# Kernel tuning notes

Measured on AMD Instinct MI355X. Metric: run time of the kernel, lower is better.

The kernel has to match this reference:

```python
import jax, jax.numpy as jnp
import numpy as np

B, NS, NT, C = 32, 1000, 100, 256
LAMBDA_GIOU, LAMBDA_L1 = 10.0, 1.0


def _lsa(cost):
    """Hungarian / Jonker-Volgenant shortest-augmenting-path (numpy, O(n^2 m)).
    Matches scipy.optimize.linear_sum_assignment for rectangular matrices."""
    cost = np.asarray(cost, dtype=np.float64)
    transposed = cost.shape[0] > cost.shape[1]
    if transposed:
        cost = cost.T
    n, m = cost.shape  # n <= m
    INF = np.inf
    u = np.zeros(n + 1)
    v = np.zeros(m + 1)
    p = np.zeros(m + 1, dtype=np.int64)   # p[j] = row (1-based) assigned to col j
    way = np.zeros(m + 1, dtype=np.int64)
    for i in range(1, n + 1):
        p[0] = i
        j0 = 0
        minv = np.full(m + 1, INF)
        used = np.zeros(m + 1, dtype=bool)
        while True:
            used[j0] = True
            i0 = p[j0]
            cur = cost[i0 - 1, :] - u[i0] - v[1:]
            free = ~used[1:]
            better = free & (cur < minv[1:])
            minv[1:][better] = cur[better]
            way[1:][better] = j0
            masked = np.where(free, minv[1:], INF)
            j1 = int(np.argmin(masked)) + 1
            delta = masked[j1 - 1]
            u[p[used]] += delta
            v[used] -= delta
            minv[~used] -= delta
            j0 = j1
            if p[j0] == 0:
                break
        while j0:
            j1 = way[j0]
            p[j0] = p[j1]
            j0 = j1
    rows = p[1:] - 1
    cols = np.arange(m)
    keep = rows >= 0
    rows, cols = rows[keep], cols[keep]
    if transposed:
        rows, cols = cols, rows
    order = np.argsort(rows)
    return rows[order], cols[order]


def _pairwise_cost(logits, classes, sb, tb):
    """Per-batch (Ns,Nt) cost = CE(logits_s, class_t) + 10*(1-GIoU(box_s, box_t)) + L1mean."""
    Bc, Ns, Cd = logits.shape
    Nt = classes.shape[1]
    # Cross entropy: logsumexp over classes minus logit at target class (identical
    # math to the torch expand+flatten CE, without the Ns*Nt*C copy).
    lse = jax.nn.logsumexp(logits, axis=-1)  # (B,Ns)
    picked = jnp.take_along_axis(
        logits, jnp.broadcast_to(classes[:, None, :], (Bc, Ns, Nt)), axis=2)  # (B,Ns,Nt)
    ce = lse[:, :, None] - picked
    # Pairwise GIoU (boxes in xyxy)
    s = sb[:, :, None, :]  # (B,Ns,1,4)
    t = tb[:, None, :, :]  # (B,1,Nt,4)
    ix1 = jnp.maximum(s[..., 0], t[..., 0])
    iy1 = jnp.maximum(s[..., 1], t[..., 1])
    ix2 = jnp.minimum(s[..., 2], t[..., 2])
    iy2 = jnp.minimum(s[..., 3], t[..., 3])
    inter = jnp.clip(ix2 - ix1, 0.0) * jnp.clip(iy2 - iy1, 0.0)
    area_s = (s[..., 2] - s[..., 0]) * (s[..., 3] - s[..., 1])
    area_t = (t[..., 2] - t[..., 0]) * (t[..., 3] - t[..., 1])
    union = area_s + area_t - inter
    iou = inter / union
    cx1 = jnp.minimum(s[..., 0], t[..., 0])
    cy1 = jnp.minimum(s[..., 1], t[..., 1])
    cx2 = jnp.maximum(s[..., 2], t[..., 2])
    cy2 = jnp.maximum(s[..., 3], t[..., 3])
    carea = (cx2 - cx1) * (cy2 - cy1)
    giou = iou - (carea - union) / carea
    l1 = jnp.abs(s - t).mean(axis=-1)  # (B,Ns,Nt)
    return ce + LAMBDA_GIOU * (1.0 - giou) + LAMBDA_L1 * l1


def _valid_boxes(key, b, n):
    p = jax.random.uniform(key, (b, n, 2, 2), dtype=jnp.float32)
    lo = p.min(axis=2)
    hi = p.max(axis=2)
    return jnp.concatenate([lo, hi], axis=-1)  # (b,n,4) xyxy, x1<x2, y1<y2


def setup_inputs() -> dict:
    key = jax.random.key(0)
    k1, k2, k3, k4 = jax.random.split(key, 4)
    return {
        "source_class_logits": jax.random.normal(k1, (B, NS, C), dtype=jnp.float32),
        "target_classes": jax.random.randint(k2, (B, NT), 0, C, dtype=jnp.int32),
        "source_boxes": _valid_boxes(k3, B, NS),
        "target_boxes": _valid_boxes(k4, B, NT),
    }


def reference(source_class_logits, target_classes, source_boxes, target_boxes):
    cost = _pairwise_cost(source_class_logits, target_classes, source_boxes, target_boxes)
    cost_np = np.asarray(cost)
    rows_l, cols_l = [], []
    for b in range(cost_np.shape[0]):  # assignment is inherently per-matrix / host-side
        r, c = _lsa(cost_np[b])
        rows_l.append(r)
        cols_l.append(c)
    rows = jnp.asarray(np.stack(rows_l))  # (B, min(Ns,Nt))
    cols = jnp.asarray(np.stack(cols_l))
    bidx = jnp.arange(cost.shape[0])[:, None]
    return cost[bidx, rows, cols].mean(axis=1)  # (B,)
```

## Files before the change

kernel.cpp:

```cpp
#include <hip/hip_runtime.h>
#include <math.h>

#define NSRC 1000
#define NTGT 100
#define NCLS 256
#define NB   32
#define NSP  1024
#define PAD_IDX(j) ((j) + ((j) >> 4))
#define LDSN (NSP + (NSP >> 4))

__global__ __launch_bounds__(256) void lse_kernel(const float* __restrict__ logits,
                                                  float* __restrict__ lse) {
    int wid  = threadIdx.x >> 6;
    int lane = threadIdx.x & 63;
    int row0 = blockIdx.x * 32 + wid * 8;
    #pragma unroll 2
    for (int r = 0; r < 8; ++r) {
        int row = row0 + r;
        float4 v4 = reinterpret_cast<const float4*>(logits + (size_t)row * NCLS)[lane];
        float m = fmaxf(fmaxf(v4.x, v4.y), fmaxf(v4.z, v4.w));
        #pragma unroll
        for (int off = 32; off >= 1; off >>= 1) m = fmaxf(m, __shfl_xor(m, off));
        float s = expf(v4.x - m) + expf(v4.y - m) + expf(v4.z - m) + expf(v4.w - m);
        #pragma unroll
        for (int off = 32; off >= 1; off >>= 1) s += __shfl_xor(s, off);
        if (lane == 0) lse[row] = m + logf(s);
    }
}

__global__ __launch_bounds__(256) void cost_kernel(const float* __restrict__ logits,
                                                   const int*   __restrict__ tcls,
                                                   const float* __restrict__ sbox,
                                                   const float* __restrict__ tbox,
                                                   const float* __restrict__ lse,
                                                   float*       __restrict__ cost,
                                                   float*       __restrict__ urow_g,
                                                   int*         __restrict__ jmin_g) {
    int b  = blockIdx.x & 31;
    int t  = blockIdx.x >> 5;
    int bt = b * NTGT + t;
    int cls = tcls[bt];
    float4 tb = reinterpret_cast<const float4*>(tbox)[bt];
    float area_t = (tb.z - tb.x) * (tb.w - tb.y);
    float* crow = cost + (size_t)bt * NSP;
    float m = 1e38f; int mi = 0x7fffffff;
    for (int s = threadIdx.x; s < NSP; s += 256) {
        if (s >= NSRC) { crow[s] = 1e30f; continue; }
        int gs = b * NSRC + s;
        float4 sb = reinterpret_cast<const float4*>(sbox)[gs];
        float ce = lse[gs] - logits[(size_t)gs * NCLS + cls];
        float ix1 = fmaxf(sb.x, tb.x), iy1 = fmaxf(sb.y, tb.y);
        float ix2 = fminf(sb.z, tb.z), iy2 = fminf(sb.w, tb.w);
        float inter = fmaxf(ix2 - ix1, 0.f) * fmaxf(iy2 - iy1, 0.f);
        float area_s = (sb.z - sb.x) * (sb.w - sb.y);
        float uni = area_s + area_t - inter;
        float iou = inter / uni;
        float cx1 = fminf(sb.x, tb.x), cy1 = fminf(sb.y, tb.y);
        float cx2 = fmaxf(sb.z, tb.z), cy2 = fmaxf(sb.w, tb.w);
        float carea = (cx2 - cx1) * (cy2 - cy1);
        float giou = iou - (carea - uni) / carea;
        float l1 = 0.25f * (fabsf(sb.x - tb.x) + fabsf(sb.y - tb.y) +
                            fabsf(sb.z - tb.z) + fabsf(sb.w - tb.w));
        float c = ce + 10.0f * (1.0f - giou) + l1;
        crow[s] = c;
        if (c < m) { m = c; mi = s; }
    }
    #pragma unroll
    for (int off = 32; off >= 1; off >>= 1) {
        float om = __shfl_xor(m, off);
        int   oi = __shfl_xor(mi, off);
        if (om < m || (om == m && oi < mi)) { m = om; mi = oi; }
    }
    __shared__ float smin[4];
    __shared__ int   sidx[4];
    int wid = threadIdx.x >> 6, lane = threadIdx.x & 63;
    if (lane == 0) { smin[wid] = m; sidx[wid] = mi; }
    __syncthreads();
    if (threadIdx.x == 0) {
        #pragma unroll
        for (int w = 1; w < 4; ++w) {
            float om = smin[w]; int oi = sidx[w];
            if (om < m || (om == m && oi < mi)) { m = om; mi = oi; }
        }
        urow_g[bt] = m;
        jmin_g[bt] = mi;
    }
}

__global__ __launch_bounds__(64) void lsa_kernel(const float* __restrict__ cost,
                                                 const float* __restrict__ urow_g,
                                                 const int*   __restrict__ jmin_g,
                                                 float* __restrict__ out) {
    int b    = blockIdx.x;
    int lane = threadIdx.x;
    const float* C = cost + (size_t)b * NTGT * NSP;
    __shared__ int   way[LDSN];
    __shared__ int   pcol[LDSN];
    __shared__ float uu[LDSN];
    __shared__ float urow[NTGT];
    __shared__ int   jmin[NTGT];
    __shared__ int   done[NTGT];
    for (int t = lane; t < LDSN; t += 64) { pcol[t] = -1; uu[t] = 0.f; way[t] = 0x7fffffff; }
    for (int t = lane; t < NTGT; t += 64) {
        urow[t] = urow_g[b * NTGT + t];
        jmin[t] = jmin_g[b * NTGT + t];
    }
    float v[16], d[16];
    #pragma unroll
    for (int k = 0; k < 16; ++k) v[k] = 0.f;
    int base = lane * 16;
    __syncthreads();

    for (int r = lane; r < NTGT; r += 64) atomicMin(&way[PAD_IDX(jmin[r])], r);
    __syncthreads();
    for (int r = lane; r < NTGT; r += 64) {
        int j = jmin[r];
        int w = (way[PAD_IDX(j)] == r) ? 1 : 0;
        done[r] = w;
        if (w) { pcol[PAD_IDX(j)] = r; uu[PAD_IDX(j)] = urow[r]; }
    }
    __syncthreads();

    for (int i = 0; i < NTGT; ++i) {
        if (done[i]) continue;
        float ui = urow[i];
        {
            const float4* row4 = reinterpret_cast<const float4*>(C + (size_t)i * NSP + base);
            #pragma unroll
            for (int q = 0; q < 4; ++q) {
                float4 c4 = row4[q];
                d[4*q+0] = c4.x - ui - v[4*q+0];
                d[4*q+1] = c4.y - ui - v[4*q+1];
                d[4*q+2] = c4.z - ui - v[4*q+2];
                d[4*q+3] = c4.w - ui - v[4*q+3];
            }
        }
        #pragma unroll
        for (int k = 0; k < 16; ++k) way[PAD_IDX(base + k)] = -1;
        unsigned int used = 0;
        float Df = 0.f;
        int jf = -1;

        for (int it = 0; it < NTGT + 3; ++it) {
            float lmin = 1e38f;
            #pragma unroll
            for (int k = 0; k < 16; ++k) {
                float val = ((used >> k) & 1u) ? 1e38f : d[k];
                lmin = fminf(lmin, val);
            }
            float wmin = lmin;
            #pragma unroll
            for (int off = 32; off >= 1; off >>= 1) wmin = fminf(wmin, __shfl_xor(wmin, off));
            unsigned long long msk = __ballot(lmin == wmin);
            int src = __ffsll(msk) - 1;
            int myk = -1;
            #pragma unroll
            for (int k = 15; k >= 0; --k)
                if (!((used >> k) & 1u) && d[k] == wmin) myk = k;
            int j0 = __shfl(base + myk, src);
            if (j0 < 0) break;
            int pj0 = pcol[PAD_IDX(j0)];
            if (pj0 < 0) { Df = wmin; jf = j0; break; }
            if ((j0 >> 4) == lane) used |= 1u << (j0 & 15);
            float uref = uu[PAD_IDX(j0)];
            float sft  = wmin - uref;
            const float4* rr = reinterpret_cast<const float4*>(C + (size_t)pj0 * NSP + base);
            float cr[16];
            #pragma unroll
            for (int q = 0; q < 4; ++q) {
                float4 c4 = rr[q];
                cr[4*q+0] = c4.x; cr[4*q+1] = c4.y; cr[4*q+2] = c4.z; cr[4*q+3] = c4.w;
            }
            #pragma unroll
            for (int k = 0; k < 16; ++k) {
                float cand = sft + cr[k] - v[k];
                bool upd = (cand < d[k]) && !((used >> k) & 1u);
                if (upd) { d[k] = cand; way[PAD_IDX(base + k)] = j0; }
            }
        }

        if (jf >= 0) {
            #pragma unroll
            for (int k = 0; k < 16; ++k) {
                if ((used >> k) & 1u) {
                    float diff = Df - d[k];
                    v[k] -= diff;
                    uu[PAD_IDX(base + k)] += diff;
                }
            }
        }
        __syncthreads();
        if (lane == 0 && jf >= 0) {
            int j = jf;
            for (int g = 0; g < NSP; ++g) {
                int jp = way[PAD_IDX(j)];
                if (jp < 0) { pcol[PAD_IDX(j)] = i; uu[PAD_IDX(j)] = ui + Df; break; }
                pcol[PAD_IDX(j)] = pcol[PAD_IDX(jp)];
                uu[PAD_IDX(j)]   = uu[PAD_IDX(jp)];
                j = jp;
            }
        }
        __syncthreads();
    }

    float acc = 0.f;
    #pragma unroll
    for (int k = 0; k < 16; ++k) {
        int j = base + k;
        if (j < NSRC) {
            int r = pcol[PAD_IDX(j)];
            if (r >= 0) acc += C[(size_t)r * NSP + j];
        }
    }
    #pragma unroll
    for (int off = 32; off >= 1; off >>= 1) acc += __shfl_xor(acc, off);
    if (lane == 0) out[b] = acc * (1.0f / NTGT);
}

extern "C" void kernel_launch(void* const* d_in, const int* in_sizes, int n_in,
                              void* d_out, int out_size, void* d_ws, size_t ws_size,
                              hipStream_t stream) {
    const float* logits = (const float*)d_in[0];
    const int*   tcls   = (const int*)  d_in[1];
    const float* sbox   = (const float*)d_in[2];
    const float* tbox   = (const float*)d_in[3];
    float* out = (float*)d_out;

    float* lse    = (float*)d_ws;
    float* cost   = lse + 32768;
    float* urow_g = cost + (size_t)NB * NTGT * NSP;
    int*   jmin_g = (int*)(urow_g + NB * NTGT);

    lse_kernel <<<1000,      256, 0, stream>>>(logits, lse);
    cost_kernel<<<NB * NTGT, 256, 0, stream>>>(logits, tcls, sbox, tbox, lse, cost,
                                               urow_g, jmin_g);
    lsa_kernel <<<NB,        64,  0, stream>>>(cost, urow_g, jmin_g, out);
}
```

Baseline: 148.6 us.

## Add auction-style augmenting row reduction before shortest-path LSA phase

Adds a queue-driven augmenting row reduction pass, as in Jonker-Volgenant, after the initial column-min greedy assignment. Each unassigned row finds its best and second-best reduced cost by wavefront shuffle, takes the best column, lowers that column's price, and pushes any displaced row back onto the queue, for at most 400 steps. The aim is to assign most rows cheaply so the expensive per-row shortest augmenting path loop runs fewer times. The cost is extra serialized steps with a block barrier each, and a risk to optimality or correctness if the dual variables become inconsistent.

```diff
diff --git a/kernel.cpp b/kernel.cpp
--- a/kernel.cpp
+++ b/kernel.cpp
@@ -100,6 +100,7 @@
     __shared__ float urow[NTGT];
     __shared__ int   jmin[NTGT];
     __shared__ int   done[NTGT];
+    __shared__ int   queue[512];
     for (int t = lane; t < LDSN; t += 64) { pcol[t] = -1; uu[t] = 0.f; way[t] = 0x7fffffff; }
     for (int t = lane; t < NTGT; t += 64) {
         urow[t] = urow_g[b * NTGT + t];
@@ -118,6 +119,54 @@
         int w = (way[PAD_IDX(j)] == r) ? 1 : 0;
         done[r] = w;
         if (w) { pcol[PAD_IDX(j)] = r; uu[PAD_IDX(j)] = urow[r]; }
+    }
+    __syncthreads();
+
+    int qh = 0, qt = 0;
+    for (int r = 0; r < NTGT; ++r) {
+        if (!done[r]) { if (lane == 0) queue[qt] = r; qt++; }
+    }
+    __syncthreads();
+    int steps = 0;
+    while (qh < qt && steps < 400) {
+        ++steps;
+        int i = queue[qh++];
+        const float4* row4 = reinterpret_cast<const float4*>(C + (size_t)i * NSP + base);
+        float m1 = 1e38f, m2 = 1e38f; int j1 = 0x7fffffff;
+        #pragma unroll
+        for (int q = 0; q < 4; ++q) {
+            float4 c4 = row4[q];
+            float vals[4] = {c4.x - v[4*q+0], c4.y - v[4*q+1],
+                             c4.z - v[4*q+2], c4.w - v[4*q+3]};
+            #pragma unroll
+            for (int e = 0; e < 4; ++e) {
+                float val = vals[e];
+                if (val < m1) { m2 = m1; m1 = val; j1 = base + 4*q + e; }
+                else m2 = fminf(m2, val);
+            }
+        }
+        #pragma unroll
+        for (int off = 32; off >= 1; off >>= 1) {
+            float om1 = __shfl_xor(m1, off);
+            float om2 = __shfl_xor(m2, off);
+            int   oj1 = __shfl_xor(j1, off);
+            bool take = (om1 < m1) || (om1 == m1 && oj1 < j1);
+            float lose = take ? m1 : om1;
+            m1 = take ? om1 : m1;
+            j1 = take ? oj1 : j1;
+            m2 = fminf(fminf(m2, om2), lose);
+        }
+        int old = pcol[PAD_IDX(j1)];
+        if ((j1 >> 4) == lane) v[j1 & 15] -= (m2 - m1);
+        if (lane == 0) {
+            pcol[PAD_IDX(j1)] = i;
+            uu[PAD_IDX(j1)]   = m2;
+            urow[i] = m2;
+            done[i] = 1;
+            if (old >= 0) { queue[qt] = old; done[old] = 0; }
+        }
+        if (old >= 0) qt++;
+        __syncthreads();
     }
     __syncthreads();
 
@@ -199,6 +248,7 @@
                 uu[PAD_IDX(j)]   = uu[PAD_IDX(jp)];
                 j = jp;
             }
+            done[i] = 1;
         }
         __syncthreads();
     }
```

After: 153.8 us. +3.5%, slower.
